# Performance work log

Hardware: AMD Instinct MI355X
Metric: run time of the kernel (lower is better)

Reference implementation:

```python
import jax, jax.numpy as jnp
import numpy as np

# Llama-7B-like decode-step config (GQA)
H = 32      # query heads
HKV = 8     # kv heads
D = 128     # head dim
HID = 4096  # hidden size (= H*D)
S = 32768   # stored quantized cache length
B = 1       # batch
Q = 1       # q_len (fused SmartKV path requires q_len == 1)


def rotate_half(x):
    return jnp.concatenate([-x[..., D // 2:], x[..., :D // 2]], axis=-1)


def setup_inputs() -> dict:
    key = jax.random.key(0)
    ks = jax.random.split(key, 9)
    hidden_states = jax.random.normal(ks[0], (B, Q, HID), jnp.float32)
    # quantized KV cache: signed int codes + per-(token, kv_head) scales
    k_qx = jax.random.randint(ks[1], (S, HKV, D), -128, 128, jnp.int32)
    v_qx = jax.random.randint(ks[2], (S, HKV, D), -128, 128, jnp.int32)
    k_scale = jax.random.uniform(ks[3], (S, HKV, 1), jnp.float32, 0.005, 0.02)
    v_scale = jax.random.uniform(ks[4], (S, HKV, 1), jnp.float32, 0.005, 0.02)
    # RoPE angles for the current decode position (pos = S)
    inv_freq = 1.0 / (10000.0 ** (jnp.arange(0, D, 2).astype(jnp.float32) / D))
    ang = jnp.concatenate([S * inv_freq, S * inv_freq])  # [D]
    cos = jnp.cos(ang)
    sin = jnp.sin(ang)
    sc = 1.0 / np.sqrt(HID)
    Wq = jax.random.normal(ks[5], (HID, H * D), jnp.float32) * sc
    Wk = jax.random.normal(ks[6], (HID, HKV * D), jnp.float32) * sc
    Wv = jax.random.normal(ks[7], (HID, HKV * D), jnp.float32) * sc
    Wo = jax.random.normal(ks[8], (H * D, HID), jnp.float32) * sc
    return dict(hidden_states=hidden_states, k_qx=k_qx, k_scale=k_scale,
                v_qx=v_qx, v_scale=v_scale, cos=cos, sin=sin,
                Wq=Wq, Wk=Wk, Wv=Wv, Wo=Wo)


def reference(hidden_states, k_qx, k_scale, v_qx, v_scale, cos, sin, Wq, Wk, Wv, Wo):
    b, q_len, _ = hidden_states.shape  # b=1, q_len=1 (decode)
    G = H // HKV  # GQA group size
    # QKV projections
    q = (hidden_states @ Wq).reshape(b, q_len, H, D).transpose(0, 2, 1, 3)      # [B,H,Q,D]
    k = (hidden_states @ Wk).reshape(b, q_len, HKV, D).transpose(0, 2, 1, 3)    # [B,HKV,Q,D]
    v = (hidden_states @ Wv).reshape(b, q_len, HKV, D).transpose(0, 2, 1, 3)    # [B,HKV,Q,D]
    # RoPE on current-token q, k
    c = cos[None, None, None, :]
    s = sin[None, None, None, :]
    q = q * c + rotate_half(q) * s
    k = k * c + rotate_half(k) * s
    # inline dequantization of SmartKV cache (kept at HKV heads; GQA handled in einsum
    # instead of materializing repeat_interleave)
    Kp = k_qx.astype(jnp.float32) * k_scale  # [S,HKV,D]
    Vp = v_qx.astype(jnp.float32) * v_scale  # [S,HKV,D]
    qg = q.reshape(b, HKV, G, q_len, D)
    scale = 1.0 / jnp.sqrt(jnp.float32(D))
    s_past = jnp.einsum('bkgqd,skd->bkgqs', qg, Kp) * scale        # [B,HKV,G,Q,S]
    s_cur = jnp.einsum('bkgqd,bkqd->bkgq', qg, k)[..., None] * scale  # current token
    scores = jnp.concatenate([s_past, s_cur], axis=-1)             # [B,HKV,G,Q,S+1]
    probs = jax.nn.softmax(scores, axis=-1)
    out = (jnp.einsum('bkgqs,skd->bkgqd', probs[..., :S], Vp)
           + probs[..., S:] * v[:, :, None, :, :])                 # [B,HKV,G,Q,D]
    out = out.reshape(b, H, q_len, D).transpose(0, 2, 1, 3).reshape(b, q_len, H * D)
    return out @ Wo
```

## Files before the change

kernel.cpp:

```cpp
#include <hip/hip_runtime.h>
#include <hip/hip_bf16.h>

#define H_    32
#define HKV_  8
#define D_    128
#define HID_  4096
#define S_    32768
#define NQKV  6144
#define SPLIT 64
#define CHUNK 512
#define NCHUNK (S_ / CHUNK)
#define SCALE_ 0.08838834764831843f

#define WS_QKV_PART 0
#define WS_QKV      393216
#define WS_SCORES   399360
#define WS_BLOCKMAX 1447936
#define WS_M        1449984
#define WS_PCUR     1450016
#define WS_PV_PART  1450048
#define WS_DSUM     2498624
#define WS_ATTN     2500672
#define WS_OPART    2504768

__global__ __launch_bounds__(256) void k_qkv_part(
    const float* __restrict__ hid, const float* __restrict__ Wq,
    const float* __restrict__ Wk, const float* __restrict__ Wv,
    float* __restrict__ part)
{
    const int j0 = blockIdx.x * 1024 + threadIdx.x * 4;
    const int i0 = blockIdx.y * (HID_ / SPLIT);
    __shared__ float hs[HID_ / SPLIT];
    if (threadIdx.x < HID_ / SPLIT) hs[threadIdx.x] = hid[i0 + threadIdx.x];
    __syncthreads();

    const float* W; int ldw; int col;
    if (j0 < 4096)       { W = Wq; ldw = 4096; col = j0; }
    else if (j0 < 5120)  { W = Wk; ldw = 1024; col = j0 - 4096; }
    else                 { W = Wv; ldw = 1024; col = j0 - 5120; }

    float4 acc = {0.f, 0.f, 0.f, 0.f};
    const float* p = W + (size_t)i0 * ldw + col;
    #pragma unroll 8
    for (int i = 0; i < HID_ / SPLIT; ++i) {
        const float4 wv = *(const float4*)(p + (size_t)i * ldw);
        const float h = hs[i];
        acc.x += h * wv.x; acc.y += h * wv.y; acc.z += h * wv.z; acc.w += h * wv.w;
    }
    *(float4*)&part[(size_t)blockIdx.y * NQKV + j0] = acc;
}

__global__ __launch_bounds__(256) void k_qkv_reduce(
    const float* __restrict__ part, const float* __restrict__ cosv,
    const float* __restrict__ sinv, float* __restrict__ qkv)
{
    const int j = blockIdx.x * 256 + threadIdx.x;
    float s = 0.f;
    #pragma unroll 8
    for (int k = 0; k < SPLIT; ++k) s += part[(size_t)k * NQKV + j];
    __shared__ float buf[256];
    buf[threadIdx.x] = s;
    __syncthreads();
    float out = s;
    if (j < 5120) {
        const int d = j & 127;
        const float rot = (d < 64) ? -buf[threadIdx.x + 64] : buf[threadIdx.x - 64];
        out = s * cosv[d] + rot * sinv[d];
    }
    qkv[j] = out;
}

__global__ __launch_bounds__(256) void k_scores(
    const int* __restrict__ kqx, const float* __restrict__ kscale,
    const float* __restrict__ qkv, float* __restrict__ scores,
    float* __restrict__ blockmax)
{
    const int kh = blockIdx.y;
    const int c0 = blockIdx.x * CHUNK;
    const int tid = threadIdx.x;
    const int w = tid >> 6, l = tid & 63;
    const int t = l >> 3, j = l & 7;

    float4 qf[4][4];
    #pragma unroll
    for (int g = 0; g < 4; ++g) {
        #pragma unroll
        for (int k = 0; k < 4; ++k)
            qf[g][k] = *(const float4*)&qkv[(kh * 4 + g) * D_ + (j + 8 * k) * 4];
    }

    float mx[4] = {-1e30f, -1e30f, -1e30f, -1e30f};

    for (int it = 0; it < CHUNK / 32; ++it) {
        const int tok = c0 + it * 32 + w * 8 + t;
        const int* kp = kqx + ((size_t)tok * HKV_ + kh) * D_;
        float dot[4] = {0.f, 0.f, 0.f, 0.f};
        #pragma unroll
        for (int k = 0; k < 4; ++k) {
            const int4 kv = *(const int4*)(kp + (j + 8 * k) * 4);
            const float f0 = (float)kv.x, f1 = (float)kv.y;
            const float f2 = (float)kv.z, f3 = (float)kv.w;
            #pragma unroll
            for (int g = 0; g < 4; ++g)
                dot[g] += f0 * qf[g][k].x + f1 * qf[g][k].y +
                          f2 * qf[g][k].z + f3 * qf[g][k].w;
        }
        #pragma unroll
        for (int m = 1; m < 8; m <<= 1) {
            #pragma unroll
            for (int g = 0; g < 4; ++g) dot[g] += __shfl_xor(dot[g], m, 64);
        }
        const float sc = kscale[tok * HKV_ + kh] * SCALE_;
        #pragma unroll
        for (int g = 0; g < 4; ++g) { dot[g] *= sc; mx[g] = fmaxf(mx[g], dot[g]); }
        if (j < 4) scores[(size_t)(kh * 4 + j) * S_ + tok] = dot[j];
    }
    #pragma unroll
    for (int m = 8; m < 64; m <<= 1) {
        #pragma unroll
        for (int g = 0; g < 4; ++g) mx[g] = fmaxf(mx[g], __shfl_xor(mx[g], m, 64));
    }
    __shared__ float wmax[4][4];
    if (l == 0) {
        for (int g = 0; g < 4; ++g) wmax[w][g] = mx[g];
    }
    __syncthreads();
    if (tid < 4) {
        const float m0 = fmaxf(fmaxf(wmax[0][tid], wmax[1][tid]),
                               fmaxf(wmax[2][tid], wmax[3][tid]));
        blockmax[(kh * 4 + tid) * NCHUNK + blockIdx.x] = m0;
    }
}

__global__ __launch_bounds__(256) void k_finalize(
    const float* __restrict__ qkv, const float* __restrict__ blockmax,
    float* __restrict__ M, float* __restrict__ pcur)
{
    __shared__ float scur_s[H_];
    const int tid = threadIdx.x;
    const int h = tid >> 3, j = tid & 7;
    const float* q = qkv + h * D_;
    const float* k = qkv + 4096 + (h >> 2) * D_;
    float p = 0.f;
    #pragma unroll
    for (int e = 0; e < 16; ++e) { const int d = j * 16 + e; p += q[d] * k[d]; }
    #pragma unroll
    for (int m = 1; m < 8; m <<= 1) p += __shfl_xor(p, m, 64);
    if (j == 0) scur_s[h] = p * SCALE_;
    __syncthreads();
    if (tid < H_) {
        float m0 = scur_s[tid];
        for (int c = 0; c < NCHUNK; ++c)
            m0 = fmaxf(m0, blockmax[tid * NCHUNK + c]);
        M[tid] = m0;
        pcur[tid] = __expf(scur_s[tid] - m0);
    }
}

__global__ __launch_bounds__(256) void k_pv(
    const int* __restrict__ vqx, const float* __restrict__ vscale,
    const float* __restrict__ scores, const float* __restrict__ M,
    float* __restrict__ pv_part, float* __restrict__ dsum_part)
{
    const int kh = blockIdx.y;
    const int c0 = blockIdx.x * CHUNK;
    const int tid = threadIdx.x;
    const int w = tid >> 6, l = tid & 63;
    const int t = l >> 3, j = l & 7;

    float Mh[4];
    #pragma unroll
    for (int g = 0; g < 4; ++g) Mh[g] = M[kh * 4 + g];

    float4 acc[4][4];
    #pragma unroll
    for (int g = 0; g < 4; ++g) {
        #pragma unroll
        for (int k = 0; k < 4; ++k) acc[g][k] = make_float4(0.f, 0.f, 0.f, 0.f);
    }
    float ds[4] = {0.f, 0.f, 0.f, 0.f};

    for (int it = 0; it < CHUNK / 32; ++it) {
        const int tok = c0 + it * 32 + w * 8 + t;
        const int* vp = vqx + ((size_t)tok * HKV_ + kh) * D_;
        float wgt[4];
        #pragma unroll
        for (int g = 0; g < 4; ++g)
            wgt[g] = __expf(scores[(size_t)(kh * 4 + g) * S_ + tok] - Mh[g]);
        #pragma unroll
        for (int g = 0; g < 4; ++g) ds[g] += wgt[g];
        const float vs = vscale[tok * HKV_ + kh];
        #pragma unroll
        for (int g = 0; g < 4; ++g) wgt[g] *= vs;
        #pragma unroll
        for (int k = 0; k < 4; ++k) {
            const int4 vv = *(const int4*)(vp + (j + 8 * k) * 4);
            const float f0 = (float)vv.x, f1 = (float)vv.y;
            const float f2 = (float)vv.z, f3 = (float)vv.w;
            #pragma unroll
            for (int g = 0; g < 4; ++g) {
                acc[g][k].x += wgt[g] * f0; acc[g][k].y += wgt[g] * f1;
                acc[g][k].z += wgt[g] * f2; acc[g][k].w += wgt[g] * f3;
            }
        }
    }
    #pragma unroll
    for (int m = 8; m < 64; m <<= 1) {
        #pragma unroll
        for (int g = 0; g < 4; ++g) {
            #pragma unroll
            for (int k = 0; k < 4; ++k) {
                acc[g][k].x += __shfl_xor(acc[g][k].x, m, 64);
                acc[g][k].y += __shfl_xor(acc[g][k].y, m, 64);
                acc[g][k].z += __shfl_xor(acc[g][k].z, m, 64);
                acc[g][k].w += __shfl_xor(acc[g][k].w, m, 64);
            }
        }
        #pragma unroll
        for (int g = 0; g < 4; ++g) ds[g] += __shfl_xor(ds[g], m, 64);
    }
    __shared__ float lacc[4][8][64];
    __shared__ float ldss[4][4];
    if (t == 0) {
        #pragma unroll
        for (int g = 0; g < 4; ++g) {
            #pragma unroll
            for (int k = 0; k < 4; ++k)
                *(float4*)&lacc[w][j][g * 16 + k * 4] = acc[g][k];
        }
    }
    if (l == 0) {
        for (int g = 0; g < 4; ++g) ldss[w][g] = ds[g];
    }
    __syncthreads();
    for (int idx = tid; idx < 512; idx += 256) {
        const int g = idx >> 7, d = idx & 127;
        const int e = d & 3, jk = d >> 2, jj = jk & 7, kk = jk >> 3;
        const float v = lacc[0][jj][g * 16 + kk * 4 + e] + lacc[1][jj][g * 16 + kk * 4 + e] +
                        lacc[2][jj][g * 16 + kk * 4 + e] + lacc[3][jj][g * 16 + kk * 4 + e];
        pv_part[(((size_t)blockIdx.x * HKV_ + kh) * 4 + g) * D_ + d] = v;
    }
    if (tid < 4)
        dsum_part[(blockIdx.x * HKV_ + kh) * 4 + tid] =
            ldss[0][tid] + ldss[1][tid] + ldss[2][tid] + ldss[3][tid];
}

__global__ __launch_bounds__(256) void k_combine(
    const float* __restrict__ pv_part, const float* __restrict__ dsum_part,
    const float* __restrict__ pcur, const float* __restrict__ qkv,
    float* __restrict__ attn)
{
    const int idx = blockIdx.x * 256 + threadIdx.x;
    const int h = idx >> 7, d = idx & 127;
    const int kh = h >> 2, g = h & 3;
    float pv = 0.f;
    for (int c = 0; c < NCHUNK; ++c)
        pv += pv_part[(((size_t)c * HKV_ + kh) * 4 + g) * D_ + d];
    float dsum = 0.f;
    for (int c = 0; c < NCHUNK; ++c)
        dsum += dsum_part[(c * HKV_ + kh) * 4 + g];
    const float pc = pcur[h];
    const float vcur = qkv[5120 + kh * D_ + d];
    attn[idx] = (pv + pc * vcur) / (dsum + pc);
}

__global__ __launch_bounds__(256) void k_out_part(
    const float* __restrict__ attn, const float* __restrict__ Wo,
    float* __restrict__ opart)
{
    const int j0 = blockIdx.x * 1024 + threadIdx.x * 4;
    const int i0 = blockIdx.y * (HID_ / SPLIT);
    __shared__ float hs[HID_ / SPLIT];
    if (threadIdx.x < HID_ / SPLIT) hs[threadIdx.x] = attn[i0 + threadIdx.x];
    __syncthreads();
    float4 acc = {0.f, 0.f, 0.f, 0.f};
    const float* p = Wo + (size_t)i0 * HID_ + j0;
    #pragma unroll 8
    for (int i = 0; i < HID_ / SPLIT; ++i) {
        const float4 wv = *(const float4*)(p + (size_t)i * HID_);
        const float h = hs[i];
        acc.x += h * wv.x; acc.y += h * wv.y; acc.z += h * wv.z; acc.w += h * wv.w;
    }
    *(float4*)&opart[(size_t)blockIdx.y * HID_ + j0] = acc;
}

__global__ __launch_bounds__(256) void k_out_reduce(
    const float* __restrict__ opart, float* __restrict__ out)
{
    const int j = blockIdx.x * 256 + threadIdx.x;
    float s = 0.f;
    #pragma unroll 8
    for (int k = 0; k < SPLIT; ++k) s += opart[(size_t)k * HID_ + j];
    out[j] = s;
}

extern "C" void kernel_launch(void* const* d_in, const int* in_sizes, int n_in,
                              void* d_out, int out_size, void* d_ws, size_t ws_size,
                              hipStream_t stream) {
    const float* hid    = (const float*)d_in[0];
    const int*   kqx    = (const int*)d_in[1];
    const float* kscale = (const float*)d_in[2];
    const int*   vqx    = (const int*)d_in[3];
    const float* vscale = (const float*)d_in[4];
    const float* cosv   = (const float*)d_in[5];
    const float* sinv   = (const float*)d_in[6];
    const float* Wq     = (const float*)d_in[7];
    const float* Wk     = (const float*)d_in[8];
    const float* Wv     = (const float*)d_in[9];
    const float* Wo     = (const float*)d_in[10];
    float* ws  = (float*)d_ws;
    float* out = (float*)d_out;

    k_qkv_part  <<<dim3(6, SPLIT), 256, 0, stream>>>(hid, Wq, Wk, Wv, ws + WS_QKV_PART);
    k_qkv_reduce<<<dim3(24),       256, 0, stream>>>(ws + WS_QKV_PART, cosv, sinv, ws + WS_QKV);
    k_scores    <<<dim3(NCHUNK, HKV_), 256, 0, stream>>>(kqx, kscale, ws + WS_QKV,
                                                         ws + WS_SCORES, ws + WS_BLOCKMAX);
    k_finalize  <<<dim3(1),        256, 0, stream>>>(ws + WS_QKV, ws + WS_BLOCKMAX,
                                                     ws + WS_M, ws + WS_PCUR);
    k_pv        <<<dim3(NCHUNK, HKV_), 256, 0, stream>>>(vqx, vscale, ws + WS_SCORES,
                                                         ws + WS_M, ws + WS_PV_PART, ws + WS_DSUM);
    k_combine   <<<dim3(16),       256, 0, stream>>>(ws + WS_PV_PART, ws + WS_DSUM,
                                                     ws + WS_PCUR, ws + WS_QKV, ws + WS_ATTN);
    k_out_part  <<<dim3(4, SPLIT), 256, 0, stream>>>(ws + WS_ATTN, Wo, ws + WS_OPART);
    k_out_reduce<<<dim3(16),       256, 0, stream>>>(ws + WS_OPART, out);
}
```

Before: 122.6 us.

## Fuse scores, max and PV into single flash-decoding kernel with online softmax

Merges the score, finalize and PV kernels into one split-K flash-decoding kernel that keeps a running max per chunk, rescales its accumulators, and writes per-chunk partial outputs, sums and maxima. The combine kernel now computes the current-token score and merges the chunks with log-sum-exp rescaling. This removes the global scores round trip and two launches. It also changes SPLIT and CHUNK and adds a launch-bounds occupancy hint. The trade-off is a data-dependent rescale branch, more register pressure, and twice as many chunk partials to combine.

Result: slower. 142.1 us (+15.9%).

```diff
diff --git a/kernel.cpp b/kernel.cpp
--- a/kernel.cpp
+++ b/kernel.cpp
@@ -7,21 +7,19 @@
 #define HID_  4096
 #define S_    32768
 #define NQKV  6144
-#define SPLIT 64
-#define CHUNK 512
+#define SPLIT 128
+#define CHUNK 256
 #define NCHUNK (S_ / CHUNK)
 #define SCALE_ 0.08838834764831843f
+#define MINIT 8.0f
 
 #define WS_QKV_PART 0
-#define WS_QKV      393216
-#define WS_SCORES   399360
-#define WS_BLOCKMAX 1447936
-#define WS_M        1449984
-#define WS_PCUR     1450016
-#define WS_PV_PART  1450048
-#define WS_DSUM     2498624
-#define WS_ATTN     2500672
-#define WS_OPART    2504768
+#define WS_QKV      786432
+#define WS_PV_C     792576
+#define WS_L_C      1316864
+#define WS_M_C      1320960
+#define WS_ATTN     1325056
+#define WS_OPART    1329152
 
 __global__ __launch_bounds__(256) void k_qkv_part(
     const float* __restrict__ hid, const float* __restrict__ Wq,
@@ -70,10 +68,11 @@
     qkv[j] = out;
 }
 
-__global__ __launch_bounds__(256) void k_scores(
+__global__ __launch_bounds__(256, 2) void k_attn(
     const int* __restrict__ kqx, const float* __restrict__ kscale,
-    const float* __restrict__ qkv, float* __restrict__ scores,
-    float* __restrict__ blockmax)
+    const int* __restrict__ vqx, const float* __restrict__ vscale,
+    const float* __restrict__ qkv, float* __restrict__ pv_c,
+    float* __restrict__ l_c, float* __restrict__ m_c)
 {
     const int kh = blockIdx.y;
     const int c0 = blockIdx.x * CHUNK;
@@ -89,7 +88,14 @@
             qf[g][k] = *(const float4*)&qkv[(kh * 4 + g) * D_ + (j + 8 * k) * 4];
     }
 
-    float mx[4] = {-1e30f, -1e30f, -1e30f, -1e30f};
+    float m[4]  = {MINIT, MINIT, MINIT, MINIT};
+    float ls[4] = {0.f, 0.f, 0.f, 0.f};
+    float4 acc[4][4];
+    #pragma unroll
+    for (int g = 0; g < 4; ++g) {
+        #pragma unroll
+        for (int k = 0; k < 4; ++k) acc[g][k] = make_float4(0.f, 0.f, 0.f, 0.f);
+    }
 
     for (int it = 0; it < CHUNK / 32; ++it) {
         const int tok = c0 + it * 32 + w * 8 + t;
@@ -106,92 +112,31 @@
                           f2 * qf[g][k].z + f3 * qf[g][k].w;
         }
         #pragma unroll
-        for (int m = 1; m < 8; m <<= 1) {
-            #pragma unroll
-            for (int g = 0; g < 4; ++g) dot[g] += __shfl_xor(dot[g], m, 64);
+        for (int msk = 1; msk < 8; msk <<= 1) {
+            #pragma unroll
+            for (int g = 0; g < 4; ++g) dot[g] += __shfl_xor(dot[g], msk, 64);
         }
         const float sc = kscale[tok * HKV_ + kh] * SCALE_;
-        #pragma unroll
-        for (int g = 0; g < 4; ++g) { dot[g] *= sc; mx[g] = fmaxf(mx[g], dot[g]); }
-        if (j < 4) scores[(size_t)(kh * 4 + j) * S_ + tok] = dot[j];
-    }
-    #pragma unroll
-    for (int m = 8; m < 64; m <<= 1) {
-        #pragma unroll
-        for (int g = 0; g < 4; ++g) mx[g] = fmaxf(mx[g], __shfl_xor(mx[g], m, 64));
-    }
-    __shared__ float wmax[4][4];
-    if (l == 0) {
-        for (int g = 0; g < 4; ++g) wmax[w][g] = mx[g];
-    }
-    __syncthreads();
-    if (tid < 4) {
-        const float m0 = fmaxf(fmaxf(wmax[0][tid], wmax[1][tid]),
-                               fmaxf(wmax[2][tid], wmax[3][tid]));
-        blockmax[(kh * 4 + tid) * NCHUNK + blockIdx.x] = m0;
-    }
-}
-
-__global__ __launch_bounds__(256) void k_finalize(
-    const float* __restrict__ qkv, const float* __restrict__ blockmax,
-    float* __restrict__ M, float* __restrict__ pcur)
-{
-    __shared__ float scur_s[H_];
-    const int tid = threadIdx.x;
-    const int h = tid >> 3, j = tid & 7;
-    const float* q = qkv + h * D_;
-    const float* k = qkv + 4096 + (h >> 2) * D_;
-    float p = 0.f;
-    #pragma unroll
-    for (int e = 0; e < 16; ++e) { const int d = j * 16 + e; p += q[d] * k[d]; }
-    #pragma unroll
-    for (int m = 1; m < 8; m <<= 1) p += __shfl_xor(p, m, 64);
-    if (j == 0) scur_s[h] = p * SCALE_;
-    __syncthreads();
-    if (tid < H_) {
-        float m0 = scur_s[tid];
-        for (int c = 0; c < NCHUNK; ++c)
-            m0 = fmaxf(m0, blockmax[tid * NCHUNK + c]);
-        M[tid] = m0;
-        pcur[tid] = __expf(scur_s[tid] - m0);
-    }
-}
-
-__global__ __launch_bounds__(256) void k_pv(
-    const int* __restrict__ vqx, const float* __restrict__ vscale,
-    const float* __restrict__ scores, const float* __restrict__ M,
-    float* __restrict__ pv_part, float* __restrict__ dsum_part)
-{
-    const int kh = blockIdx.y;
-    const int c0 = blockIdx.x * CHUNK;
-    const int tid = threadIdx.x;
-    const int w = tid >> 6, l = tid & 63;
-    const int t = l >> 3, j = l & 7;
-
-    float Mh[4];
-    #pragma unroll
-    for (int g = 0; g < 4; ++g) Mh[g] = M[kh * 4 + g];
-
-    float4 acc[4][4];
-    #pragma unroll
-    for (int g = 0; g < 4; ++g) {
-        #pragma unroll
-        for (int k = 0; k < 4; ++k) acc[g][k] = make_float4(0.f, 0.f, 0.f, 0.f);
-    }
-    float ds[4] = {0.f, 0.f, 0.f, 0.f};
-
-    for (int it = 0; it < CHUNK / 32; ++it) {
-        const int tok = c0 + it * 32 + w * 8 + t;
+        const float vs = vscale[tok * HKV_ + kh];
+        float wgt[4];
+        #pragma unroll
+        for (int g = 0; g < 4; ++g) {
+            dot[g] *= sc;
+            if (dot[g] > m[g]) {
+                const float r = __expf(m[g] - dot[g]);
+                ls[g] *= r;
+                #pragma unroll
+                for (int k = 0; k < 4; ++k) {
+                    acc[g][k].x *= r; acc[g][k].y *= r;
+                    acc[g][k].z *= r; acc[g][k].w *= r;
+                }
+                m[g] = dot[g];
+            }
+            wgt[g] = __expf(dot[g] - m[g]);
+            ls[g] += wgt[g];
+            wgt[g] *= vs;
+        }
         const int* vp = vqx + ((size_t)tok * HKV_ + kh) * D_;
-        float wgt[4];
-        #pragma unroll
-        for (int g = 0; g < 4; ++g)
-            wgt[g] = __expf(scores[(size_t)(kh * 4 + g) * S_ + tok] - Mh[g]);
-        #pragma unroll
-        for (int g = 0; g < 4; ++g) ds[g] += wgt[g];
-        const float vs = vscale[tok * HKV_ + kh];
-        #pragma unroll
-        for (int g = 0; g < 4; ++g) wgt[g] *= vs;
         #pragma unroll
         for (int k = 0; k < 4; ++k) {
             const int4 vv = *(const int4*)(vp + (j + 8 * k) * 4);
@@ -204,23 +149,40 @@
             }
         }
     }
+
+    float mw[4];
     #pragma unroll
-    for (int m = 8; m < 64; m <<= 1) {
+    for (int g = 0; g < 4; ++g) {
+        mw[g] = m[g];
+        #pragma unroll
+        for (int msk = 8; msk < 64; msk <<= 1)
+            mw[g] = fmaxf(mw[g], __shfl_xor(mw[g], msk, 64));
+        const float r = __expf(m[g] - mw[g]);
+        ls[g] *= r;
+        #pragma unroll
+        for (int k = 0; k < 4; ++k) {
+            acc[g][k].x *= r; acc[g][k].y *= r;
+            acc[g][k].z *= r; acc[g][k].w *= r;
+        }
+    }
+    #pragma unroll
+    for (int msk = 8; msk < 64; msk <<= 1) {
         #pragma unroll
         for (int g = 0; g < 4; ++g) {
             #pragma unroll
             for (int k = 0; k < 4; ++k) {
-                acc[g][k].x += __shfl_xor(acc[g][k].x, m, 64);
-                acc[g][k].y += __shfl_xor(acc[g][k].y, m, 64);
-                acc[g][k].z += __shfl_xor(acc[g][k].z, m, 64);
-                acc[g][k].w += __shfl_xor(acc[g][k].w, m, 64);
+                acc[g][k].x += __shfl_xor(acc[g][k].x, msk, 64);
+                acc[g][k].y += __shfl_xor(acc[g][k].y, msk, 64);
+                acc[g][k].z += __shfl_xor(acc[g][k].z, msk, 64);
+                acc[g][k].w += __shfl_xor(acc[g][k].w, msk, 64);
             }
-        }
-        #pragma unroll
-        for (int g = 0; g < 4; ++g) ds[g] += __shfl_xor(ds[g], m, 64);
-    }
+            ls[g] += __shfl_xor(ls[g], msk, 64);
+        }
+    }
+
     __shared__ float lacc[4][8][64];
-    __shared__ float ldss[4][4];
+    __shared__ float lls[4][4];
+    __shared__ float lmw[4][4];
     if (t == 0) {
         #pragma unroll
         for (int g = 0; g < 4; ++g) {
@@ -230,38 +192,65 @@
         }
     }
     if (l == 0) {
-        for (int g = 0; g < 4; ++g) ldss[w][g] = ds[g];
-    }
-    __syncthreads();
+        for (int g = 0; g < 4; ++g) { lls[w][g] = ls[g]; lmw[w][g] = mw[g]; }
+    }
+    __syncthreads();
+
     for (int idx = tid; idx < 512; idx += 256) {
         const int g = idx >> 7, d = idx & 127;
-        const int e = d & 3, jk = d >> 2, jj = jk & 7, kk = jk >> 3;
-        const float v = lacc[0][jj][g * 16 + kk * 4 + e] + lacc[1][jj][g * 16 + kk * 4 + e] +
-                        lacc[2][jj][g * 16 + kk * 4 + e] + lacc[3][jj][g * 16 + kk * 4 + e];
-        pv_part[(((size_t)blockIdx.x * HKV_ + kh) * 4 + g) * D_ + d] = v;
-    }
-    if (tid < 4)
-        dsum_part[(blockIdx.x * HKV_ + kh) * 4 + tid] =
-            ldss[0][tid] + ldss[1][tid] + ldss[2][tid] + ldss[3][tid];
+        const int e = d & 3, jj = (d >> 2) & 7, kk = d >> 5;
+        const float mc = fmaxf(fmaxf(lmw[0][g], lmw[1][g]),
+                               fmaxf(lmw[2][g], lmw[3][g]));
+        float v = 0.f;
+        #pragma unroll
+        for (int w2 = 0; w2 < 4; ++w2)
+            v += lacc[w2][jj][g * 16 + kk * 4 + e] * __expf(lmw[w2][g] - mc);
+        pv_c[((size_t)(blockIdx.x * HKV_ + kh) * 4 + g) * D_ + d] = v;
+    }
+    if (tid < 4) {
+        const int g = tid;
+        const float mc = fmaxf(fmaxf(lmw[0][g], lmw[1][g]),
+                               fmaxf(lmw[2][g], lmw[3][g]));
+        float lsum = 0.f;
+        #pragma unroll
+        for (int w2 = 0; w2 < 4; ++w2)
+            lsum += lls[w2][g] * __expf(lmw[w2][g] - mc);
+        l_c[(blockIdx.x * HKV_ + kh) * 4 + g] = lsum;
+        m_c[(blockIdx.x * HKV_ + kh) * 4 + g] = mc;
+    }
 }
 
 __global__ __launch_bounds__(256) void k_combine(
-    const float* __restrict__ pv_part, const float* __restrict__ dsum_part,
-    const float* __restrict__ pcur, const float* __restrict__ qkv,
+    const float* __restrict__ pv_c, const float* __restrict__ l_c,
+    const float* __restrict__ m_c, const float* __restrict__ qkv,
     float* __restrict__ attn)
 {
-    const int idx = blockIdx.x * 256 + threadIdx.x;
-    const int h = idx >> 7, d = idx & 127;
+    const int tid = threadIdx.x;
+    const int gid = blockIdx.x * 256 + tid;
+    const int h = gid >> 7, d = gid & 127;
     const int kh = h >> 2, g = h & 3;
-    float pv = 0.f;
+
+    __shared__ float sred[256];
+    sred[tid] = qkv[h * D_ + d] * qkv[4096 + kh * D_ + d];
+    __syncthreads();
+    for (int s = 64; s > 0; s >>= 1) {
+        if ((tid & 127) < s) sred[tid] += sred[tid + s];
+        __syncthreads();
+    }
+    const float scur = sred[tid & 128] * SCALE_;
+
+    float M = scur;
     for (int c = 0; c < NCHUNK; ++c)
-        pv += pv_part[(((size_t)c * HKV_ + kh) * 4 + g) * D_ + d];
-    float dsum = 0.f;
-    for (int c = 0; c < NCHUNK; ++c)
-        dsum += dsum_part[(c * HKV_ + kh) * 4 + g];
-    const float pc = pcur[h];
+        M = fmaxf(M, m_c[(c * HKV_ + kh) * 4 + g]);
+    float pv = 0.f, dsum = 0.f;
+    for (int c = 0; c < NCHUNK; ++c) {
+        const float r = __expf(m_c[(c * HKV_ + kh) * 4 + g] - M);
+        pv   += r * pv_c[((size_t)(c * HKV_ + kh) * 4 + g) * D_ + d];
+        dsum += r * l_c[(c * HKV_ + kh) * 4 + g];
+    }
+    const float pc = __expf(scur - M);
     const float vcur = qkv[5120 + kh * D_ + d];
-    attn[idx] = (pv + pc * vcur) / (dsum + pc);
+    attn[gid] = (pv + pc * vcur) / (dsum + pc);
 }
 
 __global__ __launch_bounds__(256) void k_out_part(
@@ -313,14 +302,11 @@
 
     k_qkv_part  <<<dim3(6, SPLIT), 256, 0, stream>>>(hid, Wq, Wk, Wv, ws + WS_QKV_PART);
     k_qkv_reduce<<<dim3(24),       256, 0, stream>>>(ws + WS_QKV_PART, cosv, sinv, ws + WS_QKV);
-    k_scores    <<<dim3(NCHUNK, HKV_), 256, 0, stream>>>(kqx, kscale, ws + WS_QKV,
-                                                         ws + WS_SCORES, ws + WS_BLOCKMAX);
-    k_finalize  <<<dim3(1),        256, 0, stream>>>(ws + WS_QKV, ws + WS_BLOCKMAX,
-                                                     ws + WS_M, ws + WS_PCUR);
-    k_pv        <<<dim3(NCHUNK, HKV_), 256, 0, stream>>>(vqx, vscale, ws + WS_SCORES,
-                                                         ws + WS_M, ws + WS_PV_PART, ws + WS_DSUM);
-    k_combine   <<<dim3(16),       256, 0, stream>>>(ws + WS_PV_PART, ws + WS_DSUM,
-                                                     ws + WS_PCUR, ws + WS_QKV, ws + WS_ATTN);
+    k_attn      <<<dim3(NCHUNK, HKV_), 256, 0, stream>>>(kqx, kscale, vqx, vscale,
+                                                         ws + WS_QKV, ws + WS_PV_C,
+                                                         ws + WS_L_C, ws + WS_M_C);
+    k_combine   <<<dim3(16),       256, 0, stream>>>(ws + WS_PV_C, ws + WS_L_C,
+                                                     ws + WS_M_C, ws + WS_QKV, ws + WS_ATTN);
     k_out_part  <<<dim3(4, SPLIT), 256, 0, stream>>>(ws + WS_ATTN, Wo, ws + WS_OPART);
     k_out_reduce<<<dim3(16),       256, 0, stream>>>(ws + WS_OPART, out);
 }
```
